# Optimization experiments

Hardware: AMD Instinct MI355X
Metric: run time of the kernel (lower is better)

The kernel has to match this reference:

```python
import jax, jax.numpy as jnp
import numpy as np


def setup_inputs() -> dict:
    key = jax.random.key(0)
    kq, kk, kv = jax.random.split(key, 3)
    B, L, S, H, E = 2, 2048, 2048, 8, 64
    queries = jax.random.normal(kq, (B, L, H, E), dtype=jnp.float32)
    keys = jax.random.normal(kk, (B, S, H, E), dtype=jnp.float32)
    values = jax.random.normal(kv, (B, S, H, E), dtype=jnp.float32)
    a1 = jnp.float32(1.0)
    a2 = jnp.float32(1.0)
    return {"queries": queries, "keys": keys, "values": values, "a1": a1, "a2": a2}


def reference(queries, keys, values, a1, a2):
    # queries: (B,L,H,E); keys/values: (B,S,H,E)
    E = queries.shape[-1]
    scale = 1.0 / jnp.sqrt(jnp.float32(E))
    # shared QK scores: (B,H,L,S)
    qk = jnp.einsum('blhe,bshe->bhls', queries, keys) * scale
    # sparse branch: relu^2 (dropout = identity in eval)
    ssa = jnp.square(jax.nn.relu(qk))
    ssa_out = jnp.einsum('bhls,bshd->blhd', ssa, values)
    # dense branch: softmax over keys
    dsa = jax.nn.softmax(qk, axis=-1)
    dsa_out = jnp.einsum('bhls,bshd->blhd', dsa, values)
    w1 = jnp.exp(a1)
    w2 = jnp.exp(a2)
    alpha1 = w1 / (w1 + w2)
    alpha2 = w2 / (w1 + w2)
    return alpha1 * ssa_out + alpha2 * dsa_out
```

## Files before the change

### kernel.cpp

```cpp
#include <hip/hip_runtime.h>

typedef short short4v __attribute__((ext_vector_type(4)));
typedef short short8v __attribute__((ext_vector_type(8)));
typedef float float4v __attribute__((ext_vector_type(4)));
typedef unsigned short u16;

#define NB 2
#define NL 2048
#define NS 2048
#define NH 8
#define NE 64
#define HE (NH*NE)
#define NLT (NL/64)
#define NST (NS/64)
#define TILE_U16 4096
#define HTILES 16
#define PHALF ((size_t)16*32*64*64)

static __device__ __forceinline__ unsigned pk2bf(float a, float b) {
  union { float f; unsigned u; } x, y; x.f = a; y.f = b;
  return __builtin_amdgcn_perm(y.u + 0x8000u, x.u + 0x8000u, 0x07060302u);
}

#define GLD16(gp, lp) __builtin_amdgcn_global_load_lds( \
    (const __attribute__((address_space(1))) void*)(gp), \
    (__attribute__((address_space(3))) void*)(lp), 16, 0, 0)

static __device__ __forceinline__ int fK(int s) { return (s & 3) | ((s >> 1) & 4); }

__global__ __launch_bounds__(256)
void prepack(const float* __restrict__ kp, const float* __restrict__ vp,
             u16* __restrict__ kimg, u16* __restrict__ vimg)
{
  __shared__ __align__(16) u16 ldsv[TILE_U16];

  const int tile = blockIdx.x;
  const int st = tile & (NST - 1);
  const int bh = tile >> 5;
  const int h  = bh & (NH - 1);
  const int b  = bh >> 3;
  const int s0 = st * 64;
  const size_t base = (size_t)b * NS * HE + h * NE;
  const int tid  = threadIdx.x;
  const int wv   = tid >> 6;
  const int lane = tid & 63;
  const int ln7  = lane & 7;

  u16* kt = kimg + (size_t)tile * TILE_U16;
  u16* vt = vimg + (size_t)tile * TILE_U16;

  for (int slot = tid; slot < 512; slot += 256) {
    const int srow = slot >> 3, p = slot & 7, c = p ^ fK(srow);
    const float* src = kp + base + (size_t)(s0 + srow) * HE + c * 8;
    float4 x0 = *(const float4*)src;
    float4 x1 = *(const float4*)(src + 4);
    unsigned d[4] = { pk2bf(x0.x, x0.y), pk2bf(x0.z, x0.w),
                      pk2bf(x1.x, x1.y), pk2bf(x1.z, x1.w) };
    *(int4*)(kt + slot * 8) = *(const int4*)d;
  }

  {
    const float* vcol = vp + base + (size_t)(s0 + wv * 16) * HE + lane;
    unsigned vr[8];
    #pragma unroll
    for (int jj = 0; jj < 8; ++jj)
      vr[jj] = pk2bf(vcol[(size_t)(2 * jj) * HE], vcol[(size_t)(2 * jj + 1) * HE]);
    #pragma unroll
    for (int i = 0; i < 2; ++i) {
      const int cs = (2 * wv + i) ^ ln7;
      int4 t4 = make_int4((int)vr[4*i+0], (int)vr[4*i+1],
                          (int)vr[4*i+2], (int)vr[4*i+3]);
      *(int4*)(&ldsv[lane * 64 + cs * 8]) = t4;
    }
  }
  __syncthreads();
  {
    const int4* s = (const int4*)ldsv;
    int4* dst = (int4*)vt;
    dst[tid]       = s[tid];
    dst[tid + 256] = s[tid + 256];
  }
}

__global__ __launch_bounds__(256, 4)
void assa_fwd(const float* __restrict__ qp, const u16* __restrict__ kimg,
              const u16* __restrict__ vimg, float* __restrict__ Apart,
              float* __restrict__ Dpart, float* __restrict__ Lpart)
{
  __shared__ __align__(16) u16 ldsb[2][2 * TILE_U16];

  const int tid  = threadIdx.x;
  const int wv   = tid >> 6;
  const int lane = tid & 63;
  const int ln15 = lane & 15;
  const int ln7  = lane & 7;
  const int quad = lane >> 4;

  const int bid  = blockIdx.x;
  const int bh   = bid & 15;
  const int rest = bid >> 4;
  const int lt   = rest & 31;
  const int half = rest >> 5;
  const int h    = bh & (NH - 1);
  const int b    = bh >> 3;

  const int lbase = lt * 64 + wv * 16;

  short8v qf0, qf1;
  {
    const float* qrow = qp + ((size_t)(b * NL + lbase + ln15)) * HE + h * NE + quad * 8;
    float4 q0 = *(const float4*)(qrow);
    float4 q1 = *(const float4*)(qrow + 4);
    float4 q2 = *(const float4*)(qrow + 32);
    float4 q3 = *(const float4*)(qrow + 36);
    unsigned d0[4] = { pk2bf(0.125f*q0.x, 0.125f*q0.y), pk2bf(0.125f*q0.z, 0.125f*q0.w),
                       pk2bf(0.125f*q1.x, 0.125f*q1.y), pk2bf(0.125f*q1.z, 0.125f*q1.w) };
    unsigned d1[4] = { pk2bf(0.125f*q2.x, 0.125f*q2.y), pk2bf(0.125f*q2.z, 0.125f*q2.w),
                       pk2bf(0.125f*q3.x, 0.125f*q3.y), pk2bf(0.125f*q3.z, 0.125f*q3.w) };
    qf0 = *(const short8v*)d0;
    qf1 = *(const short8v*)d1;
  }

  const size_t tbase = (size_t)bh * NST + half * HTILES;

  float4v acc_s[4], acc_d[4];
  #pragma unroll
  for (int t = 0; t < 4; ++t)
    #pragma unroll
    for (int r = 0; r < 4; ++r) { acc_s[t][r] = 0.0f; acc_d[t][r] = 0.0f; }

  float l_part = 0.0f;

  auto dma_tile = [&](int ti, int nb) {
    const int hf = wv & 1;
    const u16* g;
    u16* l;
    if (wv < 2) {
      g = kimg + (tbase + ti) * TILE_U16 + hf * 2048 + lane * 8;
      l = &ldsb[nb][hf * 2048];
    } else {
      g = vimg + (tbase + ti) * TILE_U16 + hf * 2048 + lane * 8;
      l = &ldsb[nb][TILE_U16 + hf * 2048];
    }
    GLD16(g,        l);
    GLD16(g +  512, l +  512);
    GLD16(g + 1024, l + 1024);
    GLD16(g + 1536, l + 1536);
  };

  dma_tile(0, 0);

  const int rperm = 8 * (ln15 >> 2) + (ln15 & 3);
  const int fk    = (ln15 & 3) | (((ln15 >> 2) & 1) << 2);

  for (int ti = 0; ti < HTILES; ++ti) {
    __builtin_amdgcn_s_waitcnt(0);
    __syncthreads();
    if (ti + 1 < HTILES) dma_tile(ti + 1, (ti + 1) & 1);

    const u16* kb_l = ldsb[ti & 1];
    const u16* vb_l = ldsb[ti & 1] + TILE_U16;

    #pragma unroll
    for (int U = 0; U < 2; ++U) {
      float4v sa0, sa1;
      #pragma unroll
      for (int r = 0; r < 4; ++r) { sa0[r] = 0.0f; sa1[r] = 0.0f; }
      const u16* krow0 = &kb_l[(32 * U + rperm) * 64];
      const u16* krow1 = krow0 + 4 * 64;
      short8v kf00 = *(const short8v*)(krow0 + (quad ^ fk) * 8);
      short8v kf01 = *(const short8v*)(krow0 + ((4 + quad) ^ fk) * 8);
      short8v kf10 = *(const short8v*)(krow1 + (quad ^ fk) * 8);
      short8v kf11 = *(const short8v*)(krow1 + ((4 + quad) ^ fk) * 8);
      sa0 = __builtin_amdgcn_mfma_f32_16x16x32_bf16(kf00, qf0, sa0, 0, 0, 0);
      sa0 = __builtin_amdgcn_mfma_f32_16x16x32_bf16(kf01, qf1, sa0, 0, 0, 0);
      sa1 = __builtin_amdgcn_mfma_f32_16x16x32_bf16(kf10, qf0, sa1, 0, 0, 0);
      sa1 = __builtin_amdgcn_mfma_f32_16x16x32_bf16(kf11, qf1, sa1, 0, 0, 0);

      float ps[8], pd[8];
      #pragma unroll
      for (int r = 0; r < 4; ++r) {
        float s0 = sa0[r], s1 = sa1[r];
        float r0 = s0 > 0.0f ? s0 : 0.0f;
        float r1 = s1 > 0.0f ? s1 : 0.0f;
        ps[r] = r0 * r0;  ps[4 + r] = r1 * r1;
        pd[r] = __expf(s0); pd[4 + r] = __expf(s1);
        l_part += pd[r] + pd[4 + r];
      }
      unsigned da[4] = { pk2bf(ps[0], ps[1]), pk2bf(ps[2], ps[3]),
                         pk2bf(ps[4], ps[5]), pk2bf(ps[6], ps[7]) };
      unsigned db[4] = { pk2bf(pd[0], pd[1]), pk2bf(pd[2], pd[3]),
                         pk2bf(pd[4], pd[5]), pk2bf(pd[6], pd[7]) };
      short8v as8 = *(const short8v*)da;
      short8v ad8 = *(const short8v*)db;

      #pragma unroll
      for (int t = 0; t < 4; ++t) {
        short8v vf = *(const short8v*)(&vb_l[(t * 16 + ln15) * 64 +
                        (((4 * U + quad) ^ ln7) * 8)]);
        acc_s[t] = __builtin_amdgcn_mfma_f32_16x16x32_bf16(as8, vf, acc_s[t], 0, 0, 0);
        acc_d[t] = __builtin_amdgcn_mfma_f32_16x16x32_bf16(ad8, vf, acc_d[t], 0, 0, 0);
      }
    }
  }

  l_part += __shfl_xor(l_part, 16, 64);
  l_part += __shfl_xor(l_part, 32, 64);

  float* Ab = Apart + half * PHALF + (((size_t)bh * 32 + lt) * 64) * 64;
  float* Db = Dpart + half * PHALF + (((size_t)bh * 32 + lt) * 64) * 64;
  #pragma unroll
  for (int t = 0; t < 4; ++t) {
    #pragma unroll
    for (int r = 0; r < 4; ++r) {
      const int ll = wv * 16 + quad * 4 + r;
      const int e  = t * 16 + ln15;
      Ab[ll * 64 + e] = acc_s[t][r];
      Db[ll * 64 + e] = acc_d[t][r];
    }
  }
  if (quad == 0)
    Lpart[(size_t)(half * 16 + bh) * NL + lt * 64 + wv * 16 + ln15] = l_part;
}

__global__ __launch_bounds__(256)
void assa_reduce(const float* __restrict__ Apart, const float* __restrict__ Dpart,
                 const float* __restrict__ Lpart, const float* __restrict__ a1p,
                 const float* __restrict__ a2p, float* __restrict__ op)
{
  const int idx = blockIdx.x * 256 + threadIdx.x;
  const int e4 = idx & 15;
  const int h  = (idx >> 4) & 7;
  const int l  = (idx >> 7) & 2047;
  const int b  = idx >> 18;
  const int bh = b * 8 + h;
  const int lt = l >> 6, ll = l & 63;

  const size_t pbase = ((((size_t)bh * 32 + lt) * 64) + ll) * 64 + e4 * 4;
  float4 A0 = *(const float4*)(Apart + pbase);
  float4 A1 = *(const float4*)(Apart + PHALF + pbase);
  float4 D0 = *(const float4*)(Dpart + pbase);
  float4 D1 = *(const float4*)(Dpart + PHALF + pbase);
  const float l0 = Lpart[(size_t)bh * NL + l];
  const float l1 = Lpart[(size_t)(16 + bh) * NL + l];

  const float w1 = __expf(a1p[0]), w2 = __expf(a2p[0]);
  const float al1 = w1 / (w1 + w2);
  const float al2d = (w2 / (w1 + w2)) / (l0 + l1);

  float4 o;
  o.x = al1 * (A0.x + A1.x) + al2d * (D0.x + D1.x);
  o.y = al1 * (A0.y + A1.y) + al2d * (D0.y + D1.y);
  o.z = al1 * (A0.z + A1.z) + al2d * (D0.z + D1.z);
  o.w = al1 * (A0.w + A1.w) + al2d * (D0.w + D1.w);
  *(float4*)(op + (size_t)idx * 4) = o;
}

extern "C" void kernel_launch(void* const* d_in, const int* in_sizes, int n_in,
                              void* d_out, int out_size, void* d_ws, size_t ws_size,
                              hipStream_t stream) {
  const float* q  = (const float*)d_in[0];
  const float* k  = (const float*)d_in[1];
  const float* v  = (const float*)d_in[2];
  const float* a1 = (const float*)d_in[3];
  const float* a2 = (const float*)d_in[4];
  float* out = (float*)d_out;
  (void)in_sizes; (void)n_in; (void)out_size; (void)ws_size;

  u16* kimg = (u16*)d_ws;
  u16* vimg = kimg + (size_t)NB * NH * NST * TILE_U16;
  float* Apart = (float*)(vimg + (size_t)NB * NH * NST * TILE_U16);
  float* Dpart = Apart + 2 * PHALF;
  float* Lpart = Dpart + 2 * PHALF;

  prepack<<<dim3(NB * NH * NST), dim3(256), 0, stream>>>(k, v, kimg, vimg);
  assa_fwd<<<dim3(NB * NH * NLT * 2), dim3(256), 0, stream>>>(q, kimg, vimg,
                                                              Apart, Dpart, Lpart);
  assa_reduce<<<dim3(2048), dim3(256), 0, stream>>>(Apart, Dpart, Lpart, a1, a2, out);
}
```

Baseline: 118.1 us.

## Process two query tiles per block to reuse K/V LDS tiles, split prepack

```diff
diff --git a/kernel.cpp b/kernel.cpp
--- a/kernel.cpp
+++ b/kernel.cpp
@@ -11,11 +11,10 @@
 #define NH 8
 #define NE 64
 #define HE (NH*NE)
-#define NLT (NL/64)
 #define NST (NS/64)
 #define TILE_U16 4096
 #define HTILES 16
-#define PHALF ((size_t)16*32*64*64)
+#define PHALF ((size_t)16*16*128*64)
 
 static __device__ __forceinline__ unsigned pk2bf(float a, float b) {
   union { float f; unsigned u; } x, y; x.f = a; y.f = b;
@@ -34,7 +33,9 @@
 {
   __shared__ __align__(16) u16 ldsv[TILE_U16];
 
-  const int tile = blockIdx.x;
+  const int bid  = blockIdx.x;
+  const int tile = bid >> 1;
+  const int doV  = bid & 1;
   const int st = tile & (NST - 1);
   const int bh = tile >> 5;
   const int h  = bh & (NH - 1);
@@ -46,19 +47,21 @@
   const int lane = tid & 63;
   const int ln7  = lane & 7;
 
-  u16* kt = kimg + (size_t)tile * TILE_U16;
+  if (!doV) {
+    u16* kt = kimg + (size_t)tile * TILE_U16;
+    for (int slot = tid; slot < 512; slot += 256) {
+      const int srow = slot >> 3, p = slot & 7, c = p ^ fK(srow);
+      const float* src = kp + base + (size_t)(s0 + srow) * HE + c * 8;
+      float4 x0 = *(const float4*)src;
+      float4 x1 = *(const float4*)(src + 4);
+      unsigned d[4] = { pk2bf(x0.x, x0.y), pk2bf(x0.z, x0.w),
+                        pk2bf(x1.x, x1.y), pk2bf(x1.z, x1.w) };
+      *(int4*)(kt + slot * 8) = *(const int4*)d;
+    }
+    return;
+  }
+
   u16* vt = vimg + (size_t)tile * TILE_U16;
-
-  for (int slot = tid; slot < 512; slot += 256) {
-    const int srow = slot >> 3, p = slot & 7, c = p ^ fK(srow);
-    const float* src = kp + base + (size_t)(s0 + srow) * HE + c * 8;
-    float4 x0 = *(const float4*)src;
-    float4 x1 = *(const float4*)(src + 4);
-    unsigned d[4] = { pk2bf(x0.x, x0.y), pk2bf(x0.z, x0.w),
-                      pk2bf(x1.x, x1.y), pk2bf(x1.z, x1.w) };
-    *(int4*)(kt + slot * 8) = *(const int4*)d;
-  }
-
   {
     const float* vcol = vp + base + (size_t)(s0 + wv * 16) * HE + lane;
     unsigned vr[8];
@@ -82,7 +85,7 @@
   }
 }
 
-__global__ __launch_bounds__(256, 4)
+__global__ __launch_bounds__(256, 2)
 void assa_fwd(const float* __restrict__ qp, const u16* __restrict__ kimg,
               const u16* __restrict__ vimg, float* __restrict__ Apart,
               float* __restrict__ Dpart, float* __restrict__ Lpart)
@@ -99,37 +102,54 @@
   const int bid  = blockIdx.x;
   const int bh   = bid & 15;
   const int rest = bid >> 4;
-  const int lt   = rest & 31;
-  const int half = rest >> 5;
+  const int lt   = rest & 15;
+  const int half = rest >> 4;
   const int h    = bh & (NH - 1);
   const int b    = bh >> 3;
 
-  const int lbase = lt * 64 + wv * 16;
-
-  short8v qf0, qf1;
+  const int lbA = lt * 128 + wv * 16;
+  const int lbB = lbA + 64;
+
+  short8v qA0, qA1, qB0, qB1;
   {
-    const float* qrow = qp + ((size_t)(b * NL + lbase + ln15)) * HE + h * NE + quad * 8;
-    float4 q0 = *(const float4*)(qrow);
-    float4 q1 = *(const float4*)(qrow + 4);
-    float4 q2 = *(const float4*)(qrow + 32);
-    float4 q3 = *(const float4*)(qrow + 36);
+    const float* qr = qp + ((size_t)(b * NL + lbA + ln15)) * HE + h * NE + quad * 8;
+    float4 q0 = *(const float4*)(qr);
+    float4 q1 = *(const float4*)(qr + 4);
+    float4 q2 = *(const float4*)(qr + 32);
+    float4 q3 = *(const float4*)(qr + 36);
     unsigned d0[4] = { pk2bf(0.125f*q0.x, 0.125f*q0.y), pk2bf(0.125f*q0.z, 0.125f*q0.w),
                        pk2bf(0.125f*q1.x, 0.125f*q1.y), pk2bf(0.125f*q1.z, 0.125f*q1.w) };
     unsigned d1[4] = { pk2bf(0.125f*q2.x, 0.125f*q2.y), pk2bf(0.125f*q2.z, 0.125f*q2.w),
                        pk2bf(0.125f*q3.x, 0.125f*q3.y), pk2bf(0.125f*q3.z, 0.125f*q3.w) };
-    qf0 = *(const short8v*)d0;
-    qf1 = *(const short8v*)d1;
+    qA0 = *(const short8v*)d0;
+    qA1 = *(const short8v*)d1;
+  }
+  {
+    const float* qr = qp + ((size_t)(b * NL + lbB + ln15)) * HE + h * NE + quad * 8;
+    float4 q0 = *(const float4*)(qr);
+    float4 q1 = *(const float4*)(qr + 4);
+    float4 q2 = *(const float4*)(qr + 32);
+    float4 q3 = *(const float4*)(qr + 36);
+    unsigned d0[4] = { pk2bf(0.125f*q0.x, 0.125f*q0.y), pk2bf(0.125f*q0.z, 0.125f*q0.w),
+                       pk2bf(0.125f*q1.x, 0.125f*q1.y), pk2bf(0.125f*q1.z, 0.125f*q1.w) };
+    unsigned d1[4] = { pk2bf(0.125f*q2.x, 0.125f*q2.y), pk2bf(0.125f*q2.z, 0.125f*q2.w),
+                       pk2bf(0.125f*q3.x, 0.125f*q3.y), pk2bf(0.125f*q3.z, 0.125f*q3.w) };
+    qB0 = *(const short8v*)d0;
+    qB1 = *(const short8v*)d1;
   }
 
   const size_t tbase = (size_t)bh * NST + half * HTILES;
 
-  float4v acc_s[4], acc_d[4];
+  float4v aAs[4], aAd[4], aBs[4], aBd[4];
   #pragma unroll
   for (int t = 0; t < 4; ++t)
     #pragma unroll
-    for (int r = 0; r < 4; ++r) { acc_s[t][r] = 0.0f; acc_d[t][r] = 0.0f; }
-
-  float l_part = 0.0f;
+    for (int r = 0; r < 4; ++r) {
+      aAs[t][r] = 0.0f; aAd[t][r] = 0.0f;
+      aBs[t][r] = 0.0f; aBd[t][r] = 0.0f;
+    }
+
+  float lA = 0.0f, lB = 0.0f;
 
   auto dma_tile = [&](int ti, int nb) {
     const int hf = wv & 1;
@@ -163,64 +183,98 @@
 
     #pragma unroll
     for (int U = 0; U < 2; ++U) {
-      float4v sa0, sa1;
-      #pragma unroll
-      for (int r = 0; r < 4; ++r) { sa0[r] = 0.0f; sa1[r] = 0.0f; }
       const u16* krow0 = &kb_l[(32 * U + rperm) * 64];
       const u16* krow1 = krow0 + 4 * 64;
       short8v kf00 = *(const short8v*)(krow0 + (quad ^ fk) * 8);
       short8v kf01 = *(const short8v*)(krow0 + ((4 + quad) ^ fk) * 8);
       short8v kf10 = *(const short8v*)(krow1 + (quad ^ fk) * 8);
       short8v kf11 = *(const short8v*)(krow1 + ((4 + quad) ^ fk) * 8);
-      sa0 = __builtin_amdgcn_mfma_f32_16x16x32_bf16(kf00, qf0, sa0, 0, 0, 0);
-      sa0 = __builtin_amdgcn_mfma_f32_16x16x32_bf16(kf01, qf1, sa0, 0, 0, 0);
-      sa1 = __builtin_amdgcn_mfma_f32_16x16x32_bf16(kf10, qf0, sa1, 0, 0, 0);
-      sa1 = __builtin_amdgcn_mfma_f32_16x16x32_bf16(kf11, qf1, sa1, 0, 0, 0);
-
-      float ps[8], pd[8];
+
+      float4v sA0, sA1, sB0, sB1;
       #pragma unroll
-      for (int r = 0; r < 4; ++r) {
-        float s0 = sa0[r], s1 = sa1[r];
-        float r0 = s0 > 0.0f ? s0 : 0.0f;
-        float r1 = s1 > 0.0f ? s1 : 0.0f;
-        ps[r] = r0 * r0;  ps[4 + r] = r1 * r1;
-        pd[r] = __expf(s0); pd[4 + r] = __expf(s1);
-        l_part += pd[r] + pd[4 + r];
+      for (int r = 0; r < 4; ++r) { sA0[r]=0.f; sA1[r]=0.f; sB0[r]=0.f; sB1[r]=0.f; }
+      sA0 = __builtin_amdgcn_mfma_f32_16x16x32_bf16(kf00, qA0, sA0, 0, 0, 0);
+      sA0 = __builtin_amdgcn_mfma_f32_16x16x32_bf16(kf01, qA1, sA0, 0, 0, 0);
+      sA1 = __builtin_amdgcn_mfma_f32_16x16x32_bf16(kf10, qA0, sA1, 0, 0, 0);
+      sA1 = __builtin_amdgcn_mfma_f32_16x16x32_bf16(kf11, qA1, sA1, 0, 0, 0);
+      sB0 = __builtin_amdgcn_mfma_f32_16x16x32_bf16(kf00, qB0, sB0, 0, 0, 0);
+      sB0 = __builtin_amdgcn_mfma_f32_16x16x32_bf16(kf01, qB1, sB0, 0, 0, 0);
+      sB1 = __builtin_amdgcn_mfma_f32_16x16x32_bf16(kf10, qB0, sB1, 0, 0, 0);
+      sB1 = __builtin_amdgcn_mfma_f32_16x16x32_bf16(kf11, qB1, sB1, 0, 0, 0);
+
+      short8v asA, adA, asB, adB;
+      {
+        float ps[8], pd[8];
+        #pragma unroll
+        for (int r = 0; r < 4; ++r) {
+          float s0 = sA0[r], s1 = sA1[r];
+          float r0 = s0 > 0.0f ? s0 : 0.0f;
+          float r1 = s1 > 0.0f ? s1 : 0.0f;
+          ps[r] = r0 * r0;  ps[4 + r] = r1 * r1;
+          pd[r] = __expf(s0); pd[4 + r] = __expf(s1);
+          lA += pd[r] + pd[4 + r];
+        }
+        unsigned da[4] = { pk2bf(ps[0], ps[1]), pk2bf(ps[2], ps[3]),
+                           pk2bf(ps[4], ps[5]), pk2bf(ps[6], ps[7]) };
+        unsigned db[4] = { pk2bf(pd[0], pd[1]), pk2bf(pd[2], pd[3]),
+                           pk2bf(pd[4], pd[5]), pk2bf(pd[6], pd[7]) };
+        asA = *(const short8v*)da;
+        adA = *(const short8v*)db;
       }
-      unsigned da[4] = { pk2bf(ps[0], ps[1]), pk2bf(ps[2], ps[3]),
-                         pk2bf(ps[4], ps[5]), pk2bf(ps[6], ps[7]) };
-      unsigned db[4] = { pk2bf(pd[0], pd[1]), pk2bf(pd[2], pd[3]),
-                         pk2bf(pd[4], pd[5]), pk2bf(pd[6], pd[7]) };
-      short8v as8 = *(const short8v*)da;
-      short8v ad8 = *(const short8v*)db;
+      {
+        float ps[8], pd[8];
+        #pragma unroll
+        for (int r = 0; r < 4; ++r) {
+          float s0 = sB0[r], s1 = sB1[r];
+          float r0 = s0 > 0.0f ? s0 : 0.0f;
+          float r1 = s1 > 0.0f ? s1 : 0.0f;
+          ps[r] = r0 * r0;  ps[4 + r] = r1 * r1;
+          pd[r] = __expf(s0); pd[4 + r] = __expf(s1);
+          lB += pd[r] + pd[4 + r];
+        }
+        unsigned da[4] = { pk2bf(ps[0], ps[1]), pk2bf(ps[2], ps[3]),
+                           pk2bf(ps[4], ps[5]), pk2bf(ps[6], ps[7]) };
+        unsigned db[4] = { pk2bf(pd[0], pd[1]), pk2bf(pd[2], pd[3]),
+                           pk2bf(pd[4], pd[5]), pk2bf(pd[6], pd[7]) };
+        asB = *(const short8v*)da;
+        adB = *(const short8v*)db;
+      }
 
       #pragma unroll
       for (int t = 0; t < 4; ++t) {
         short8v vf = *(const short8v*)(&vb_l[(t * 16 + ln15) * 64 +
                         (((4 * U + quad) ^ ln7) * 8)]);
-        acc_s[t] = __builtin_amdgcn_mfma_f32_16x16x32_bf16(as8, vf, acc_s[t], 0, 0, 0);
-        acc_d[t] = __builtin_amdgcn_mfma_f32_16x16x32_bf16(ad8, vf, acc_d[t], 0, 0, 0);
+        aAs[t] = __builtin_amdgcn_mfma_f32_16x16x32_bf16(asA, vf, aAs[t], 0, 0, 0);
+        aAd[t] = __builtin_amdgcn_mfma_f32_16x16x32_bf16(adA, vf, aAd[t], 0, 0, 0);
+        aBs[t] = __builtin_amdgcn_mfma_f32_16x16x32_bf16(asB, vf, aBs[t], 0, 0, 0);
+        aBd[t] = __builtin_amdgcn_mfma_f32_16x16x32_bf16(adB, vf, aBd[t], 0, 0, 0);
       }
     }
   }
 
-  l_part += __shfl_xor(l_part, 16, 64);
-  l_part += __shfl_xor(l_part, 32, 64);
-
-  float* Ab = Apart + half * PHALF + (((size_t)bh * 32 + lt) * 64) * 64;
-  float* Db = Dpart + half * PHALF + (((size_t)bh * 32 + lt) * 64) * 64;
+  lA += __shfl_xor(lA, 16, 64);
+  lA += __shfl_xor(lA, 32, 64);
+  lB += __shfl_xor(lB, 16, 64);
+  lB += __shfl_xor(lB, 32, 64);
+
+  float* Ab = Apart + half * PHALF + ((size_t)(bh * 16 + lt) * 128) * 64;
+  float* Db = Dpart + half * PHALF + ((size_t)(bh * 16 + lt) * 128) * 64;
   #pragma unroll
   for (int t = 0; t < 4; ++t) {
     #pragma unroll
     for (int r = 0; r < 4; ++r) {
-      const int ll = wv * 16 + quad * 4 + r;
-      const int e  = t * 16 + ln15;
-      Ab[ll * 64 + e] = acc_s[t][r];
-      Db[ll * 64 + e] = acc_d[t][r];
-    }
-  }
-  if (quad == 0)
-    Lpart[(size_t)(half * 16 + bh) * NL + lt * 64 + wv * 16 + ln15] = l_part;
+      const int llA = wv * 16 + quad * 4 + r;
+      const int e   = t * 16 + ln15;
+      Ab[llA * 64 + e]        = aAs[t][r];
+      Db[llA * 64 + e]        = aAd[t][r];
+      Ab[(llA + 64) * 64 + e] = aBs[t][r];
+      Db[(llA + 64) * 64 + e] = aBd[t][r];
+    }
+  }
+  if (quad == 0) {
+    Lpart[(size_t)(half * 16 + bh) * NL + lbA + ln15] = lA;
+    Lpart[(size_t)(half * 16 + bh) * NL + lbB + ln15] = lB;
+  }
 }
 
 __global__ __launch_bounds__(256)
@@ -228,19 +282,22 @@
                  const float* __restrict__ Lpart, const float* __restrict__ a1p,
                  const float* __restrict__ a2p, float* __restrict__ op)
 {
-  const int idx = blockIdx.x * 256 + threadIdx.x;
-  const int e4 = idx & 15;
-  const int h  = (idx >> 4) & 7;
-  const int l  = (idx >> 7) & 2047;
-  const int b  = idx >> 18;
-  const int bh = b * 8 + h;
-  const int lt = l >> 6, ll = l & 63;
-
-  const size_t pbase = ((((size_t)bh * 32 + lt) * 64) + ll) * 64 + e4 * 4;
-  float4 A0 = *(const float4*)(Apart + pbase);
-  float4 A1 = *(const float4*)(Apart + PHALF + pbase);
-  float4 D0 = *(const float4*)(Dpart + pbase);
-  float4 D1 = *(const float4*)(Dpart + PHALF + pbase);
+  const int bid   = blockIdx.x;
+  const int bh    = bid & 15;
+  const int rest  = bid >> 4;
+  const int lt    = rest & 15;
+  const int slice = rest >> 4;
+  const int tid   = threadIdx.x;
+  const int ll    = slice * 16 + (tid >> 4);
+  const int e0    = (tid & 15) * 4;
+  const int h = bh & 7, b = bh >> 3;
+  const int l = lt * 128 + ll;
+
+  const size_t pb = ((size_t)(bh * 16 + lt) * 128 + ll) * 64 + e0;
+  float4 A0 = *(const float4*)(Apart + pb);
+  float4 A1 = *(const float4*)(Apart + PHALF + pb);
+  float4 D0 = *(const float4*)(Dpart + pb);
+  float4 D1 = *(const float4*)(Dpart + PHALF + pb);
   const float l0 = Lpart[(size_t)bh * NL + l];
   const float l1 = Lpart[(size_t)(16 + bh) * NL + l];
 
@@ -253,7 +310,7 @@
   o.y = al1 * (A0.y + A1.y) + al2d * (D0.y + D1.y);
   o.z = al1 * (A0.z + A1.z) + al2d * (D0.z + D1.z);
   o.w = al1 * (A0.w + A1.w) + al2d * (D0.w + D1.w);
-  *(float4*)(op + (size_t)idx * 4) = o;
+  *(float4*)(op + ((size_t)(b * NL + l)) * HE + h * NE + e0) = o;
 }
 
 extern "C" void kernel_launch(void* const* d_in, const int* in_sizes, int n_in,
@@ -273,8 +330,7 @@
   float* Dpart = Apart + 2 * PHALF;
   float* Lpart = Dpart + 2 * PHALF;
 
-  prepack<<<dim3(NB * NH * NST), dim3(256), 0, stream>>>(k, v, kimg, vimg);
-  assa_fwd<<<dim3(NB * NH * NLT * 2), dim3(256), 0, stream>>>(q, kimg, vimg,
-                                                              Apart, Dpart, Lpart);
+  prepack<<<dim3(NB * NH * NST * 2), dim3(256), 0, stream>>>(k, v, kimg, vimg);
+  assa_fwd<<<dim3(512), dim3(256), 0, stream>>>(q, kimg, vimg, Apart, Dpart, Lpart);
   assa_reduce<<<dim3(2048), dim3(256), 0, stream>>>(Apart, Dpart, Lpart, a1, a2, out);
 }
```

New measurement: 121.8 us. 3.1% more time.
